# Kernel optimization log

Hardware: AMD Instinct MI355X
Metric: run time of the kernel (lower is better)

## Reference

```python
import jax, jax.numpy as jnp
import numpy as np


def _cal_similarity(query, respond):
    # query: [B, n1, d], respond: [B, n2, d]
    # scores[b, c, q, r] = <query[b, q], respond[c, r]>
    scores = jnp.einsum('bqd,crd->bcqr', query, respond)  # [B, B, n1, n2]
    # max over respond tokens, mean over query tokens -> [B, B]
    return scores.max(axis=-1).mean(axis=-1)


def _ce_with_arange_labels(logits):
    # cross-entropy with labels = arange(B), mean reduction
    logp = jax.nn.log_softmax(logits, axis=-1)
    return -jnp.mean(jnp.diagonal(logp))


def setup_inputs() -> dict:
    key = jax.random.key(0)
    k1, k2 = jax.random.split(key)
    B, n1, n2, d = 96, 196, 77, 512
    image_out = jax.random.normal(k1, (B, n1, d), dtype=jnp.float32)
    text_out = jax.random.normal(k2, (B, n2, d), dtype=jnp.float32)
    return {"image_out": image_out, "text_out": text_out}


def reference(image_out, text_out):
    i2t = _cal_similarity(image_out, text_out)  # [B, B]
    t2i = _cal_similarity(text_out, image_out)  # [B, B]
    return 0.5 * (_ce_with_arange_labels(i2t) + _ce_with_arange_labels(t2i))
```

## Files before the change

### kernel.cpp

```cpp
#include <hip/hip_runtime.h>
#include <math.h>

#define BB 96
#define N1 196
#define N2 77
#define DD 512

#define IMGN (BB * N1 * DD)
#define TXTN (BB * N2 * DD)

#define ATILES 13
#define NTILES 24
#define BUFH (NTILES * 512)

typedef _Float16 f16x8 __attribute__((ext_vector_type(8)));
typedef float f4v __attribute__((ext_vector_type(4)));

typedef unsigned int __attribute__((address_space(1))) as1_uint;
typedef unsigned int __attribute__((address_space(3))) as3_uint;

__device__ __forceinline__ void gload_lds16(const void* g, void* l) {
    __builtin_amdgcn_global_load_lds((const as1_uint*)g, (as3_uint*)l, 16, 0, 0);
}

__global__ void convert_kernel(const float* __restrict__ img,
                               const float* __restrict__ txt,
                               _Float16* __restrict__ dst) {
    int i = (blockIdx.x * blockDim.x + threadIdx.x) * 4;
    if (i >= IMGN + TXTN) return;
    const float* src = (i < IMGN) ? (img + i) : (txt + (i - IMGN));
    float4 v = *(const float4*)src;
    union { _Float16 h[4]; uint2 u; } o;
    o.h[0] = (_Float16)v.x; o.h[1] = (_Float16)v.y;
    o.h[2] = (_Float16)v.z; o.h[3] = (_Float16)v.w;
    *(uint2*)(dst + i) = o.u;
}

template <int SG0, int NS, int H>
__device__ __forceinline__ void compute_sub(const f16x8* __restrict__ fr,
                                            f4v* __restrict__ acc, int lane) {
    f16x8 b[5];
#pragma unroll
    for (int ct = 0; ct < 5; ++ct)
        b[ct] = fr[(ATILES + H * 5 + ct) * 64 + lane];
#pragma unroll
    for (int i = 0; i < NS; ++i) {
        f16x8 a = fr[(SG0 + i) * 64 + lane];
#pragma unroll
        for (int ct = 0; ct < 5; ++ct)
            acc[i * 5 + ct] = __builtin_amdgcn_mfma_f32_16x16x32_f16(
                a, b[ct], acc[i * 5 + ct], 0, 0, 0);
    }
}

template <int SG0, int NS, int H>
__device__ __forceinline__ void reduce_phase1(const f4v* __restrict__ acc,
                                              int g, int lq, int lm,
                                              float* __restrict__ rp,
                                              float* __restrict__ cp) {
    float colm[5];
#pragma unroll
    for (int ct = 0; ct < 5; ++ct) colm[ct] = -INFINITY;
#pragma unroll
    for (int i = 0; i < NS; ++i) {
        const int s = SG0 + i;
        float rowm[4] = {-INFINITY, -INFINITY, -INFINITY, -INFINITY};
        bool rows_ok = (s != 12) || (lq == 0);
#pragma unroll
        for (int ct = 0; ct < 5; ++ct) {
            f4v a = acc[i * 5 + ct];
            bool col_ok = (ct != 4) || (lm < N2 - 64);
            float cm = fmaxf(fmaxf(a[0], a[1]), fmaxf(a[2], a[3]));
            colm[ct] = fmaxf(colm[ct], rows_ok ? cm : -INFINITY);
#pragma unroll
            for (int r = 0; r < 4; ++r)
                rowm[r] = fmaxf(rowm[r], col_ok ? a[r] : -INFINITY);
        }
#pragma unroll
        for (int r = 0; r < 4; ++r) {
            float m = rowm[r];
            m = fmaxf(m, __shfl_xor(m, 1));
            m = fmaxf(m, __shfl_xor(m, 2));
            m = fmaxf(m, __shfl_xor(m, 4));
            m = fmaxf(m, __shfl_xor(m, 8));
            if (lm == 0) rp[H * 208 + s * 16 + lq * 4 + r] = m;
        }
    }
#pragma unroll
    for (int ct = 0; ct < 5; ++ct) {
        float m = colm[ct];
        m = fmaxf(m, __shfl_xor(m, 16));
        m = fmaxf(m, __shfl_xor(m, 32));
        if (lq == 0) cp[g * 160 + H * 80 + ct * 16 + lm] = m;
    }
}

template <bool PRE>
__global__ __launch_bounds__(512, 4) void sim_mfma_kernel(
    const float* __restrict__ imgF, const float* __restrict__ txtF,
    const _Float16* __restrict__ h16,
    float* __restrict__ i2t, float* __restrict__ t2i)
{
    const int id  = blockIdx.x;
    const int xcd = id & 7;
    const int lid = id >> 3;
    const int w   = lid % 48;
    const int btq = lid / 48;
    const int btp = btq * 4 + (w & 3);
    const int bi  = xcd * 12 + (w >> 2);
    const int bt0 = btp * 2;

    const int tid = threadIdx.x;
    const int wave = tid >> 6, lane = tid & 63;
    const int lm = lane & 15;
    const int lq = lane >> 4;
    const int g = wave >> 1;

    __shared__ __align__(16) _Float16 lds[3 * BUFH];
    float* rp   = (float*)lds;
    float* cp   = (float*)lds + 416;
    float* sws  = (float*)lds + 1056;
    float* scol = (float*)lds + 1064;

    int off[3];
    const float* fsrc[3];
#pragma unroll
    for (int j = 0; j < 3; ++j) {
        const int T = 8 * j + wave;
        int o;
        bool isA = true;
        if (T < ATILES) {
            int q = T * 16 + lm; q = q > (N1 - 1) ? (N1 - 1) : q;
            o = (bi * N1 + q) * DD + lq * 8;
        } else if (T < 23) {
            isA = false;
            int ct = T - ATILES;
            int bt = bt0 + (ct >= 5);
            int r = (ct % 5) * 16 + lm; r = r > (N2 - 1) ? (N2 - 1) : r;
            o = (bt * N2 + r) * DD + lq * 8;
        } else {
            o = lq * 8;
        }
        if constexpr (PRE) {
            off[j] = isA ? o : (IMGN + o);
        } else {
            off[j] = o;
            fsrc[j] = isA ? imgF : txtF;
        }
    }

    auto stage = [&](int kc, int b) {
        const int k0 = kc * 32;
#pragma unroll
        for (int j = 0; j < 3; ++j)
            gload_lds16(h16 + off[j] + k0,
                        lds + (b * NTILES + 8 * j + wave) * 512);
    };

    f4v acc[20];
#pragma unroll
    for (int i = 0; i < 20; ++i) acc[i] = (f4v){0.f, 0.f, 0.f, 0.f};

    auto do_compute = [&](const f16x8* fr) {
        if (wave == 0)      compute_sub<0, 4, 0>(fr, acc, lane);
        else if (wave == 1) compute_sub<0, 4, 1>(fr, acc, lane);
        else if (wave == 2) compute_sub<4, 3, 0>(fr, acc, lane);
        else if (wave == 3) compute_sub<4, 3, 1>(fr, acc, lane);
        else if (wave == 4) compute_sub<7, 3, 0>(fr, acc, lane);
        else if (wave == 5) compute_sub<7, 3, 1>(fr, acc, lane);
        else if (wave == 6) compute_sub<10, 3, 0>(fr, acc, lane);
        else                compute_sub<10, 3, 1>(fr, acc, lane);
    };

    if constexpr (PRE) {
        stage(0, 0);
        stage(1, 1);
#pragma unroll 1
        for (int kc = 0; kc < 16; ++kc) {
            if (kc < 14) {
                stage(kc + 2, (kc + 2) % 3);
                asm volatile("s_waitcnt vmcnt(6)" ::: "memory");
            } else if (kc == 14) {
                asm volatile("s_waitcnt vmcnt(3)" ::: "memory");
            } else {
                asm volatile("s_waitcnt vmcnt(0)" ::: "memory");
            }
            __builtin_amdgcn_s_barrier();
            asm volatile("" ::: "memory");
            do_compute((const f16x8*)(lds + (kc % 3) * BUFH));
            asm volatile("" ::: "memory");
            __builtin_amdgcn_s_barrier();
        }
    } else {
#pragma unroll 1
        for (int kc = 0; kc < 16; ++kc) {
            __syncthreads();
            const int k0 = kc * 32;
#pragma unroll
            for (int j = 0; j < 3; ++j) {
                const int T = 8 * j + wave;
                if (T < 23) {
                    float4 v0 = *(const float4*)(fsrc[j] + off[j] + k0);
                    float4 v1 = *(const float4*)(fsrc[j] + off[j] + k0 + 4);
                    union { f16x8 f; uint4 u; } o;
                    o.f[0] = (_Float16)v0.x; o.f[1] = (_Float16)v0.y;
                    o.f[2] = (_Float16)v0.z; o.f[3] = (_Float16)v0.w;
                    o.f[4] = (_Float16)v1.x; o.f[5] = (_Float16)v1.y;
                    o.f[6] = (_Float16)v1.z; o.f[7] = (_Float16)v1.w;
                    ((uint4*)lds)[T * 64 + lane] = o.u;
                }
            }
            __syncthreads();
            do_compute((const f16x8*)lds);
        }
        __syncthreads();
    }

    if (wave == 0)      reduce_phase1<0, 4, 0>(acc, g, lq, lm, rp, cp);
    else if (wave == 1) reduce_phase1<0, 4, 1>(acc, g, lq, lm, rp, cp);
    else if (wave == 2) reduce_phase1<4, 3, 0>(acc, g, lq, lm, rp, cp);
    else if (wave == 3) reduce_phase1<4, 3, 1>(acc, g, lq, lm, rp, cp);
    else if (wave == 4) reduce_phase1<7, 3, 0>(acc, g, lq, lm, rp, cp);
    else if (wave == 5) reduce_phase1<7, 3, 1>(acc, g, lq, lm, rp, cp);
    else if (wave == 6) reduce_phase1<10, 3, 0>(acc, g, lq, lm, rp, cp);
    else                reduce_phase1<10, 3, 1>(acc, g, lq, lm, rp, cp);
    __syncthreads();

    {
        const int half = tid >> 8;
        const int t = tid & 255;
        float v = (t < N1) ? rp[half * 208 + t] : 0.f;
        v += __shfl_xor(v, 1);  v += __shfl_xor(v, 2);  v += __shfl_xor(v, 4);
        v += __shfl_xor(v, 8);  v += __shfl_xor(v, 16); v += __shfl_xor(v, 32);
        if (lane == 0) sws[wave] = v;
    }
    if (tid < 160) {
        float m = fmaxf(fmaxf(cp[tid], cp[160 + tid]),
                        fmaxf(cp[320 + tid], cp[480 + tid]));
        scol[tid] = m;
    }
    __syncthreads();
    if (tid == 0)
        i2t[bi * BB + bt0] =
            (sws[0] + sws[1] + sws[2] + sws[3]) * (1.f / (float)N1);
    if (tid == 1)
        i2t[bi * BB + bt0 + 1] =
            (sws[4] + sws[5] + sws[6] + sws[7]) * (1.f / (float)N1);
    if (wave < 2) {
        const float* c = scol + wave * 80;
        float cv = c[lane] + ((lane < N2 - 64) ? c[64 + lane] : 0.f);
        cv += __shfl_xor(cv, 1);  cv += __shfl_xor(cv, 2);  cv += __shfl_xor(cv, 4);
        cv += __shfl_xor(cv, 8);  cv += __shfl_xor(cv, 16); cv += __shfl_xor(cv, 32);
        if (lane == 0)
            t2i[(bt0 + wave) * BB + bi] = cv * (1.f / (float)N2);
    }
}

__global__ __launch_bounds__(256) void ce_kernel(
    const float* __restrict__ i2t, const float* __restrict__ t2i,
    float* __restrict__ out)
{
    const int tid = threadIdx.x;
    const int wid = tid >> 6;
    const int lane = tid & 63;

    float contrib = 0.f;
    if (tid < 2 * BB) {
        const float* M = (tid < BB) ? i2t : t2i;
        const int b = (tid < BB) ? tid : tid - BB;
        const float* row = M + b * BB;
        float mx = row[0];
#pragma unroll 1
        for (int c = 1; c < BB; ++c) mx = fmaxf(mx, row[c]);
        float s = 0.f;
#pragma unroll 1
        for (int c = 0; c < BB; ++c) s += expf(row[c] - mx);
        float lse = mx + logf(s);
        contrib = row[b] - lse;
    }
    contrib += __shfl_xor(contrib, 1);
    contrib += __shfl_xor(contrib, 2);
    contrib += __shfl_xor(contrib, 4);
    contrib += __shfl_xor(contrib, 8);
    contrib += __shfl_xor(contrib, 16);
    contrib += __shfl_xor(contrib, 32);

    __shared__ float s_part[4];
    if (lane == 0) s_part[wid] = contrib;
    __syncthreads();
    if (tid == 0) {
        float total = s_part[0] + s_part[1] + s_part[2] + s_part[3];
        out[0] = -total * (1.f / (float)(2 * BB));
    }
}

extern "C" void kernel_launch(void* const* d_in, const int* in_sizes, int n_in,
                              void* d_out, int out_size, void* d_ws, size_t ws_size,
                              hipStream_t stream) {
    const float* img = (const float*)d_in[0];
    const float* txt = (const float*)d_in[1];
    float* i2t = (float*)d_ws;
    float* t2i = i2t + BB * BB;

    const size_t conv_off = 2 * BB * BB * sizeof(float);
    const size_t need = conv_off + (size_t)(IMGN + TXTN) * sizeof(_Float16);

    const int nblocks = BB * (BB / 2);
    if (ws_size >= need) {
        _Float16* h16 = (_Float16*)((char*)d_ws + conv_off);
        const int ntot = (IMGN + TXTN) / 4;
        convert_kernel<<<(ntot + 255) / 256, 256, 0, stream>>>(img, txt, h16);
        sim_mfma_kernel<true><<<nblocks, 512, 0, stream>>>(img, txt, h16, i2t, t2i);
    } else {
        sim_mfma_kernel<false><<<nblocks, 512, 0, stream>>>(img, txt, nullptr, i2t, t2i);
    }
    ce_kernel<<<1, 256, 0, stream>>>(i2t, t2i, (float*)d_out);
}
```

Baseline: 308.1 us.

## Halve block to four waves with larger per-wave MFMA tiles

Shrinks the similarity kernel from 8 to 4 waves per block. Each wave now stages six LDS tiles per k-chunk and computes 6–7 query tiles against the text tiles, using 35 accumulators instead of 20. The reduction scratch moves into the third LDS buffer, and the final row and column reductions are adjusted for two wave-groups. The aim is more operand reuse per wave and fewer barrier participants, at the cost of higher register pressure and fewer resident waves to hide latency.

```diff
diff --git a/kernel.cpp b/kernel.cpp
--- a/kernel.cpp
+++ b/kernel.cpp
@@ -96,7 +96,7 @@
 }
 
 template <bool PRE>
-__global__ __launch_bounds__(512, 4) void sim_mfma_kernel(
+__global__ __launch_bounds__(256, 2) void sim_mfma_kernel(
     const float* __restrict__ imgF, const float* __restrict__ txtF,
     const _Float16* __restrict__ h16,
     float* __restrict__ i2t, float* __restrict__ t2i)
@@ -117,16 +117,17 @@
     const int g = wave >> 1;
 
     __shared__ __align__(16) _Float16 lds[3 * BUFH];
-    float* rp   = (float*)lds;
-    float* cp   = (float*)lds + 416;
-    float* sws  = (float*)lds + 1056;
-    float* scol = (float*)lds + 1064;
-
-    int off[3];
-    const float* fsrc[3];
-#pragma unroll
-    for (int j = 0; j < 3; ++j) {
-        const int T = 8 * j + wave;
+    float* scratch = (float*)(lds + 2 * BUFH);
+    float* rp   = scratch;
+    float* cp   = scratch + 416;
+    float* sws  = scratch + 736;
+    float* scol = scratch + 740;
+
+    int off[6];
+    const float* fsrc[6];
+#pragma unroll
+    for (int j = 0; j < 6; ++j) {
+        const int T = 4 * j + wave;
         int o;
         bool isA = true;
         if (T < ATILES) {
@@ -152,24 +153,20 @@
     auto stage = [&](int kc, int b) {
         const int k0 = kc * 32;
 #pragma unroll
-        for (int j = 0; j < 3; ++j)
+        for (int j = 0; j < 6; ++j)
             gload_lds16(h16 + off[j] + k0,
-                        lds + (b * NTILES + 8 * j + wave) * 512);
+                        lds + (b * NTILES + 4 * j + wave) * 512);
     };
 
-    f4v acc[20];
-#pragma unroll
-    for (int i = 0; i < 20; ++i) acc[i] = (f4v){0.f, 0.f, 0.f, 0.f};
+    f4v acc[35];
+#pragma unroll
+    for (int i = 0; i < 35; ++i) acc[i] = (f4v){0.f, 0.f, 0.f, 0.f};
 
     auto do_compute = [&](const f16x8* fr) {
-        if (wave == 0)      compute_sub<0, 4, 0>(fr, acc, lane);
-        else if (wave == 1) compute_sub<0, 4, 1>(fr, acc, lane);
-        else if (wave == 2) compute_sub<4, 3, 0>(fr, acc, lane);
-        else if (wave == 3) compute_sub<4, 3, 1>(fr, acc, lane);
-        else if (wave == 4) compute_sub<7, 3, 0>(fr, acc, lane);
-        else if (wave == 5) compute_sub<7, 3, 1>(fr, acc, lane);
-        else if (wave == 6) compute_sub<10, 3, 0>(fr, acc, lane);
-        else                compute_sub<10, 3, 1>(fr, acc, lane);
+        if (wave == 0)      compute_sub<0, 7, 0>(fr, acc, lane);
+        else if (wave == 1) compute_sub<0, 7, 1>(fr, acc, lane);
+        else if (wave == 2) compute_sub<7, 6, 0>(fr, acc, lane);
+        else                compute_sub<7, 6, 1>(fr, acc, lane);
     };
 
     if constexpr (PRE) {
@@ -179,9 +176,9 @@
         for (int kc = 0; kc < 16; ++kc) {
             if (kc < 14) {
                 stage(kc + 2, (kc + 2) % 3);
+                asm volatile("s_waitcnt vmcnt(12)" ::: "memory");
+            } else if (kc == 14) {
                 asm volatile("s_waitcnt vmcnt(6)" ::: "memory");
-            } else if (kc == 14) {
-                asm volatile("s_waitcnt vmcnt(3)" ::: "memory");
             } else {
                 asm volatile("s_waitcnt vmcnt(0)" ::: "memory");
             }
@@ -197,8 +194,8 @@
             __syncthreads();
             const int k0 = kc * 32;
 #pragma unroll
-            for (int j = 0; j < 3; ++j) {
-                const int T = 8 * j + wave;
+            for (int j = 0; j < 6; ++j) {
+                const int T = 4 * j + wave;
                 if (T < 23) {
                     float4 v0 = *(const float4*)(fsrc[j] + off[j] + k0);
                     float4 v1 = *(const float4*)(fsrc[j] + off[j] + k0 + 4);
@@ -216,36 +213,29 @@
         __syncthreads();
     }
 
-    if (wave == 0)      reduce_phase1<0, 4, 0>(acc, g, lq, lm, rp, cp);
-    else if (wave == 1) reduce_phase1<0, 4, 1>(acc, g, lq, lm, rp, cp);
-    else if (wave == 2) reduce_phase1<4, 3, 0>(acc, g, lq, lm, rp, cp);
-    else if (wave == 3) reduce_phase1<4, 3, 1>(acc, g, lq, lm, rp, cp);
-    else if (wave == 4) reduce_phase1<7, 3, 0>(acc, g, lq, lm, rp, cp);
-    else if (wave == 5) reduce_phase1<7, 3, 1>(acc, g, lq, lm, rp, cp);
-    else if (wave == 6) reduce_phase1<10, 3, 0>(acc, g, lq, lm, rp, cp);
-    else                reduce_phase1<10, 3, 1>(acc, g, lq, lm, rp, cp);
+    if (wave == 0)      reduce_phase1<0, 7, 0>(acc, g, lq, lm, rp, cp);
+    else if (wave == 1) reduce_phase1<0, 7, 1>(acc, g, lq, lm, rp, cp);
+    else if (wave == 2) reduce_phase1<7, 6, 0>(acc, g, lq, lm, rp, cp);
+    else                reduce_phase1<7, 6, 1>(acc, g, lq, lm, rp, cp);
     __syncthreads();
 
     {
-        const int half = tid >> 8;
-        const int t = tid & 255;
-        float v = (t < N1) ? rp[half * 208 + t] : 0.f;
+        const int h = wave & 1;
+        const int sseg = wave >> 1;
+        const int qa = sseg * 128 + lane;
+        const int qb = qa + 64;
+        float v = rp[h * 208 + qa];
+        if (qb < N1) v += rp[h * 208 + qb];
         v += __shfl_xor(v, 1);  v += __shfl_xor(v, 2);  v += __shfl_xor(v, 4);
         v += __shfl_xor(v, 8);  v += __shfl_xor(v, 16); v += __shfl_xor(v, 32);
         if (lane == 0) sws[wave] = v;
     }
-    if (tid < 160) {
-        float m = fmaxf(fmaxf(cp[tid], cp[160 + tid]),
-                        fmaxf(cp[320 + tid], cp[480 + tid]));
-        scol[tid] = m;
-    }
+    if (tid < 160) scol[tid] = fmaxf(cp[tid], cp[160 + tid]);
     __syncthreads();
     if (tid == 0)
-        i2t[bi * BB + bt0] =
-            (sws[0] + sws[1] + sws[2] + sws[3]) * (1.f / (float)N1);
+        i2t[bi * BB + bt0] = (sws[0] + sws[2]) * (1.f / (float)N1);
     if (tid == 1)
-        i2t[bi * BB + bt0 + 1] =
-            (sws[4] + sws[5] + sws[6] + sws[7]) * (1.f / (float)N1);
+        i2t[bi * BB + bt0 + 1] = (sws[1] + sws[3]) * (1.f / (float)N1);
     if (wave < 2) {
         const float* c = scol + wave * 80;
         float cv = c[lane] + ((lane < N2 - 64) ? c[64 + lane] : 0.f);
@@ -310,9 +300,9 @@
         _Float16* h16 = (_Float16*)((char*)d_ws + conv_off);
         const int ntot = (IMGN + TXTN) / 4;
         convert_kernel<<<(ntot + 255) / 256, 256, 0, stream>>>(img, txt, h16);
-        sim_mfma_kernel<true><<<nblocks, 512, 0, stream>>>(img, txt, h16, i2t, t2i);
+        sim_mfma_kernel<true><<<nblocks, 256, 0, stream>>>(img, txt, h16, i2t, t2i);
     } else {
-        sim_mfma_kernel<false><<<nblocks, 512, 0, stream>>>(img, txt, nullptr, i2t, t2i);
+        sim_mfma_kernel<false><<<nblocks, 256, 0, stream>>>(img, txt, nullptr, i2t, t2i);
     }
     ce_kernel<<<1, 256, 0, stream>>>(i2t, t2i, (float*)d_out);
 }
```

Result: no change. 306.2 us (-0.6%).

## Pre-tile fp16 conversion into contiguous MFMA fragment layout for LDS loads

Applied to the files above, without the earlier changes.

The conversion kernel now writes fp16 data in a tiled layout. Each 16-row by 32-k tile is stored as one contiguous 1 KB block in fragment order, with padded rows clamped. The similarity kernel's direct-to-LDS loads then read fully contiguous 1 KB chunks per wave instead of strided 64-byte row segments, which should improve global memory coalescing. In exchange, the converted buffer grows slightly because of the padding, and the converter uses more index arithmetic.

```diff
diff --git a/kernel.cpp b/kernel.cpp
--- a/kernel.cpp
+++ b/kernel.cpp
@@ -13,6 +13,10 @@
 #define NTILES 24
 #define BUFH (NTILES * 512)
 
+#define TA_TILES (BB * 13 * 16)
+#define TB_TILES (BB * 5 * 16)
+#define NT_TILES (TA_TILES + TB_TILES)
+
 typedef _Float16 f16x8 __attribute__((ext_vector_type(8)));
 typedef float f4v __attribute__((ext_vector_type(4)));
 
@@ -23,17 +27,39 @@
     __builtin_amdgcn_global_load_lds((const as1_uint*)g, (as3_uint*)l, 16, 0, 0);
 }
 
-__global__ void convert_kernel(const float* __restrict__ img,
-                               const float* __restrict__ txt,
-                               _Float16* __restrict__ dst) {
-    int i = (blockIdx.x * blockDim.x + threadIdx.x) * 4;
-    if (i >= IMGN + TXTN) return;
-    const float* src = (i < IMGN) ? (img + i) : (txt + (i - IMGN));
-    float4 v = *(const float4*)src;
-    union { _Float16 h[4]; uint2 u; } o;
-    o.h[0] = (_Float16)v.x; o.h[1] = (_Float16)v.y;
-    o.h[2] = (_Float16)v.z; o.h[3] = (_Float16)v.w;
-    *(uint2*)(dst + i) = o.u;
+__global__ void convert_tiled_kernel(const float* __restrict__ img,
+                                     const float* __restrict__ txt,
+                                     _Float16* __restrict__ dst) {
+    const int tid = blockIdx.x * blockDim.x + threadIdx.x;
+    if (tid >= NT_TILES * 64) return;
+    const int t     = tid >> 6;
+    const int cp    = tid & 63;
+    const int row16 = cp >> 2;
+    const int k8    = cp & 3;
+    const float* src;
+    if (t < TA_TILES) {
+        const int kc = t & 15;
+        const int s  = (t >> 4) % 13;
+        const int bi = t / (13 * 16);
+        int q = s * 16 + row16; q = q > (N1 - 1) ? (N1 - 1) : q;
+        src = img + (size_t)(bi * N1 + q) * DD + kc * 32 + k8 * 8;
+    } else {
+        const int tt = t - TA_TILES;
+        const int kc = tt & 15;
+        const int ct = (tt >> 4) % 5;
+        const int bt = tt / (5 * 16);
+        int r = ct * 16 + row16; r = r > (N2 - 1) ? (N2 - 1) : r;
+        src = txt + (size_t)(bt * N2 + r) * DD + kc * 32 + k8 * 8;
+    }
+    float4 v0 = *(const float4*)src;
+    float4 v1 = *(const float4*)(src + 4);
+    union { _Float16 h[8]; uint4 u; } o;
+    o.h[0] = (_Float16)v0.x; o.h[1] = (_Float16)v0.y;
+    o.h[2] = (_Float16)v0.z; o.h[3] = (_Float16)v0.w;
+    o.h[4] = (_Float16)v1.x; o.h[5] = (_Float16)v1.y;
+    o.h[6] = (_Float16)v1.z; o.h[7] = (_Float16)v1.w;
+    const int c = k8 * 16 + row16;
+    *(uint4*)(dst + (size_t)t * 512 + c * 8) = o.u;
 }
 
 template <int SG0, int NS, int H>
@@ -127,30 +153,40 @@
 #pragma unroll
     for (int j = 0; j < 3; ++j) {
         const int T = 8 * j + wave;
-        int o;
-        bool isA = true;
-        if (T < ATILES) {
-            int q = T * 16 + lm; q = q > (N1 - 1) ? (N1 - 1) : q;
-            o = (bi * N1 + q) * DD + lq * 8;
-        } else if (T < 23) {
-            isA = false;
-            int ct = T - ATILES;
-            int bt = bt0 + (ct >= 5);
-            int r = (ct % 5) * 16 + lm; r = r > (N2 - 1) ? (N2 - 1) : r;
-            o = (bt * N2 + r) * DD + lq * 8;
+        if constexpr (PRE) {
+            int t;
+            if (T < ATILES) {
+                t = (bi * 13 + T) * 16;
+            } else if (T < 23) {
+                const int ct = T - ATILES;
+                const int bt = bt0 + (ct >= 5);
+                t = TA_TILES + (bt * 5 + (ct % 5)) * 16;
+            } else {
+                t = 0;
+            }
+            off[j] = t * 512 + lane * 8;
         } else {
-            o = lq * 8;
-        }
-        if constexpr (PRE) {
-            off[j] = isA ? o : (IMGN + o);
-        } else {
+            int o;
+            bool isA = true;
+            if (T < ATILES) {
+                int q = T * 16 + lm; q = q > (N1 - 1) ? (N1 - 1) : q;
+                o = (bi * N1 + q) * DD + lq * 8;
+            } else if (T < 23) {
+                isA = false;
+                int ct = T - ATILES;
+                int bt = bt0 + (ct >= 5);
+                int r = (ct % 5) * 16 + lm; r = r > (N2 - 1) ? (N2 - 1) : r;
+                o = (bt * N2 + r) * DD + lq * 8;
+            } else {
+                o = lq * 8;
+            }
             off[j] = o;
             fsrc[j] = isA ? imgF : txtF;
         }
     }
 
     auto stage = [&](int kc, int b) {
-        const int k0 = kc * 32;
+        const int k0 = kc * 512;
 #pragma unroll
         for (int j = 0; j < 3; ++j)
             gload_lds16(h16 + off[j] + k0,
@@ -303,13 +339,13 @@
     float* t2i = i2t + BB * BB;
 
     const size_t conv_off = 2 * BB * BB * sizeof(float);
-    const size_t need = conv_off + (size_t)(IMGN + TXTN) * sizeof(_Float16);
+    const size_t need = conv_off + (size_t)NT_TILES * 512 * sizeof(_Float16);
 
     const int nblocks = BB * (BB / 2);
     if (ws_size >= need) {
         _Float16* h16 = (_Float16*)((char*)d_ws + conv_off);
-        const int ntot = (IMGN + TXTN) / 4;
-        convert_kernel<<<(ntot + 255) / 256, 256, 0, stream>>>(img, txt, h16);
+        const int nthr = NT_TILES * 64;
+        convert_tiled_kernel<<<(nthr + 255) / 256, 256, 0, stream>>>(img, txt, h16);
         sim_mfma_kernel<true><<<nblocks, 512, 0, stream>>>(img, txt, h16, i2t, t2i);
     } else {
         sim_mfma_kernel<false><<<nblocks, 512, 0, stream>>>(img, txt, nullptr, i2t, t2i);
```

Result: faster. 286.1 us (-7.1%).
